# Kernel optimization log

Measured on AMD Instinct MI355X. Metric: run time of the kernel, lower is better.

The kernel has to match this reference:

```python
import jax, jax.numpy as jnp
import numpy as np


def setup_inputs() -> dict:
    key = jax.random.key(0)
    k1, k2, k3 = jax.random.split(key, 3)
    B, C, H, W = 16, 512, 64, 64
    K = 32
    std = 1.0 / (K * C) ** 0.5
    x = jax.random.normal(k1, (B, C, H, W), dtype=jnp.float32)
    codewords = jax.random.uniform(k2, (K, C), dtype=jnp.float32, minval=-std, maxval=std)
    scale = jax.random.uniform(k3, (K,), dtype=jnp.float32, minval=-1.0, maxval=0.0)
    return {"x": x, "codewords": codewords, "scale": scale}


def reference(x, codewords, scale):
    # x: [B, C, H, W] -> tokens [B, N, C] with N = H*W
    B, C, H, W = x.shape
    xf = x.reshape(B, C, H * W).transpose(0, 2, 1)  # [B, N, C]

    # (avoids materializing the [B, N, K, C] tensor the torch code builds)
    x_sq = jnp.sum(xf * xf, axis=-1)                 # [B, N]
    c_sq = jnp.sum(codewords * codewords, axis=-1)   # [K]
    xc = jnp.einsum('bnc,kc->bnk', xf, codewords)    # [B, N, K]
    scaled_l2 = scale * (x_sq[..., None] - 2.0 * xc + c_sq)  # [B, N, K]

    w = jax.nn.softmax(scaled_l2, axis=2)            # [B, N, K]

    # aggregate: sum_n w[b,n,k] * (x[b,n,:] - c[k,:])
    #          = einsum(w, x) - (sum_n w) * c
    enc = jnp.einsum('bnk,bnc->bkc', w, xf) - jnp.sum(w, axis=1)[..., None] * codewords
    return enc  # [B, K, C]
```

## Files before the change

### kernel.cpp

```cpp
#include <hip/hip_runtime.h>


#define B_ 16
#define C_ 512
#define N_ 4096
#define K_ 32
#define CHUNK 128
#define NCH (N_ / CHUNK)
#define NBLK (B_ * NCH)
#define WLS 40

typedef __attribute__((ext_vector_type(8))) short short8;
typedef __attribute__((ext_vector_type(16))) float floatx16;

__device__ inline unsigned short f2bf(float f) {
    union { float f; unsigned u; } v; v.f = f;
    unsigned r = v.u + 0x7FFFu + ((v.u >> 16) & 1u);
    return (unsigned short)(r >> 16);
}

__device__ inline void cbar() {
    __builtin_amdgcn_sched_barrier(0);
    asm volatile("s_waitcnt lgkmcnt(0)" ::: "memory");
    __builtin_amdgcn_s_barrier();
    __builtin_amdgcn_sched_barrier(0);
}

template <int USE_WS>
__global__ __launch_bounds__(256, 3)
void enc_kernel(const float* __restrict__ x,
                const float* __restrict__ cw,
                const float* __restrict__ scale,
                float* __restrict__ outp)
{
    __shared__ unsigned short Wl[4][K_ * WLS];
    __shared__ float csq[K_];
    __shared__ float scl[K_];

    const int tid  = threadIdx.x;
    const int wave = tid >> 6;
    const int lane = tid & 63;
    const int l31  = lane & 31;
    const int lh   = lane >> 5;

    const int b     = blockIdx.x >> 5;
    const int chunk = blockIdx.x & (NCH - 1);
    const float* xb = x + (long)b * C_ * N_;

    if (tid < K_) scl[tid] = scale[tid];
    {
        const int k = tid >> 3, q = tid & 7;
        const float4* src = (const float4*)(cw + k * C_ + q * 64);
        float ssum = 0.f;
        #pragma unroll
        for (int i = 0; i < 16; ++i) {
            const float4 v = src[i];
            ssum += v.x*v.x + v.y*v.y + v.z*v.z + v.w*v.w;
        }
        ssum += __shfl_xor(ssum, 1);
        ssum += __shfl_xor(ssum, 2);
        ssum += __shfl_xor(ssum, 4);
        if (q == 0) csq[k] = ssum;
    }

    const float* xcol = xb + chunk * CHUNK + wave * 32 + l31;
    const float* cwr  = cw + l31 * C_ + lh * 8;

    short8 afA[4], afB[4];
#define AFLOADG(buf_, ptr_)                                                    \
    { _Pragma("unroll")                                                        \
      for (int s = 0; s < 4; ++s) {                                            \
          const float4 u0 = *(const float4*)((ptr_) + s * 16);                 \
          const float4 u1 = *(const float4*)((ptr_) + s * 16 + 4);             \
          short8 t_;                                                           \
          t_[0] = (short)f2bf(u0.x); t_[1] = (short)f2bf(u0.y);                \
          t_[2] = (short)f2bf(u0.z); t_[3] = (short)f2bf(u0.w);                \
          t_[4] = (short)f2bf(u1.x); t_[5] = (short)f2bf(u1.y);                \
          t_[6] = (short)f2bf(u1.z); t_[7] = (short)f2bf(u1.w);                \
          buf_[s] = t_; } }

    floatx16 S;
    #pragma unroll
    for (int i = 0; i < 16; ++i) S[i] = 0.f;
    float xs = 0.f;

    AFLOADG(afA, cwr)
    #pragma unroll 2
    for (int g = 0; g < 8; ++g) {
        const float* xg = xcol + (long)g * 64 * N_;
        if (g + 1 < 8) {
            if (g & 1) AFLOADG(afA, cwr + (g + 1) * 64)
            else       AFLOADG(afB, cwr + (g + 1) * 64)
        }
        #pragma unroll
        for (int s = 0; s < 4; ++s) {
            float xv[8];
            #pragma unroll
            for (int j = 0; j < 8; ++j)
                xv[j] = xg[(long)(s * 16 + lh * 8 + j) * N_];
            short8 bx;
            #pragma unroll
            for (int j = 0; j < 8; ++j) {
                xs += xv[j] * xv[j];
                bx[j] = (short)f2bf(xv[j]);
            }
            S = __builtin_amdgcn_mfma_f32_32x32x16_bf16(
                    (g & 1) ? afB[s] : afA[s], bx, S, 0, 0, 0);
        }
    }

    xs += __shfl_xor(xs, 32);

    float4 bv[6][2];
#define G2LOAD(bi_, i_)                                                        \
    { const int t_ = (i_) >> 3, st_ = (i_) & 7;                                \
      const int c_ = wave * 128 + t_ * 32 + l31;                               \
      const int no_ = (st_ >> 1) * 32 + (st_ & 1) * 16 + lh * 8;               \
      const float* p_ = xb + (long)c_ * N_ + chunk * CHUNK + no_;              \
      bv[bi_][0] = *(const float4*)p_;                                         \
      bv[bi_][1] = *(const float4*)(p_ + 4); }
    G2LOAD(0, 0)
    G2LOAD(1, 1)
    G2LOAD(2, 2)
    G2LOAD(3, 3)
    G2LOAD(4, 4)
    G2LOAD(5, 5)

    cbar();

    {
        const float xq = xs;
        float L[16], mx = -3.4e38f;
        #pragma unroll
        for (int rr = 0; rr < 16; ++rr) {
            const int k = (rr & 3) + 8 * (rr >> 2) + 4 * lh;
            L[rr] = scl[k] * (xq - 2.f * S[rr] + csq[k]);
            mx = fmaxf(mx, L[rr]);
        }
        mx = fmaxf(mx, __shfl_xor(mx, 32));
        float sum = 0.f;
        #pragma unroll
        for (int rr = 0; rr < 16; ++rr) { L[rr] = __expf(L[rr] - mx); sum += L[rr]; }
        sum += __shfl_xor(sum, 32);
        const float inv = 1.f / sum;
        #pragma unroll
        for (int rr = 0; rr < 16; ++rr) {
            const int k = (rr & 3) + 8 * (rr >> 2) + 4 * lh;
            Wl[wave][k * WLS + l31] = f2bf(L[rr] * inv);
        }
    }
    cbar();

    short8 aw[8];
    #pragma unroll
    for (int st = 0; st < 8; ++st)
        aw[st] = *(const short8*)&Wl[st >> 1][l31 * WLS + (st & 1) * 16 + lh * 8];

    floatx16 wacc;
    #pragma unroll
    for (int i = 0; i < 16; ++i) wacc[i] = 0.f;
    {
        short8 ones;
        #pragma unroll
        for (int j = 0; j < 8; ++j) ones[j] = (short)0x3F80;
        #pragma unroll
        for (int st = 0; st < 8; ++st)
            wacc = __builtin_amdgcn_mfma_f32_32x32x16_bf16(aw[st], ones, wacc, 0, 0, 0);
    }

    floatx16 acc[4];
    #pragma unroll
    for (int t = 0; t < 4; ++t)
        #pragma unroll
        for (int i = 0; i < 16; ++i) acc[t][i] = 0.f;

    #pragma unroll
    for (int i = 0; i < 32; ++i) {
        const int bi = i % 6;
        const int t  = i >> 3, st = i & 7;
        const float4 v0 = bv[bi][0];
        const float4 v1 = bv[bi][1];
        short8 bx;
        bx[0] = (short)f2bf(v0.x); bx[1] = (short)f2bf(v0.y);
        bx[2] = (short)f2bf(v0.z); bx[3] = (short)f2bf(v0.w);
        bx[4] = (short)f2bf(v1.x); bx[5] = (short)f2bf(v1.y);
        bx[6] = (short)f2bf(v1.z); bx[7] = (short)f2bf(v1.w);
        acc[t] = __builtin_amdgcn_mfma_f32_32x32x16_bf16(aw[st], bx, acc[t], 0, 0, 0);
        if (i + 6 < 32) G2LOAD(bi, i + 6)
    }

    float* dst = USE_WS ? (outp + (size_t)blockIdx.x * K_ * C_)
                        : (outp + (size_t)b * K_ * C_);
    #pragma unroll
    for (int t = 0; t < 4; ++t) {
        const int c = wave * 128 + t * 32 + l31;
        #pragma unroll
        for (int rr = 0; rr < 16; ++rr) {
            const int k = (rr & 3) + 8 * (rr >> 2) + 4 * lh;
            const float val = acc[t][rr] - wacc[rr] * cw[k * C_ + c];
            if (USE_WS) dst[k * C_ + c] = val;
            else        atomicAdd(dst + k * C_ + c, val);
        }
    }
}

__global__ __launch_bounds__(256)
void reduce_kernel(const float4* __restrict__ part, float4* __restrict__ out)
{
    const int gid = blockIdx.x * 256 + threadIdx.x;
    const int bb  = gid >> 12;
    const int i4  = gid & 4095;
    const float4* pp = part + ((size_t)bb * NCH) * 4096 + i4;
    float4 s = make_float4(0.f, 0.f, 0.f, 0.f);
    #pragma unroll
    for (int j = 0; j < NCH; ++j) {
        const float4 v = pp[(size_t)j * 4096];
        s.x += v.x; s.y += v.y; s.z += v.z; s.w += v.w;
    }
    out[gid] = s;
}

extern "C" void kernel_launch(void* const* d_in, const int* in_sizes, int n_in,
                              void* d_out, int out_size, void* d_ws, size_t ws_size,
                              hipStream_t stream) {
    const float* x     = (const float*)d_in[0];
    const float* cw    = (const float*)d_in[1];
    const float* scale = (const float*)d_in[2];
    float* out = (float*)d_out;

    const size_t ws_need = (size_t)NBLK * K_ * C_ * sizeof(float);
    if (ws_size >= ws_need) {
        float* part = (float*)d_ws;
        hipLaunchKernelGGL(enc_kernel<1>, dim3(NBLK), dim3(256), 0, stream,
                           x, cw, scale, part);
        hipLaunchKernelGGL(reduce_kernel, dim3(256), dim3(256), 0, stream,
                           (const float4*)part, (float4*)out);
    } else {
        hipMemsetAsync(out, 0, (size_t)out_size * sizeof(float), stream);
        hipLaunchKernelGGL(enc_kernel<0>, dim3(NBLK), dim3(256), 0, stream,
                           x, cw, scale, out);
    }
}
```

Measured before the change: 223.3 us.

## Stage x slabs through double-buffered LDS with async global_load_lds

Replaces the per-lane strided scalar global loads of x in the distance GEMM phase with async global_load_lds transfers of 64-channel slabs into a double-buffered shared-memory buffer. An explicit vmcnt wait plus barriers overlaps fetching the next slab with the MFMA work on the current one. The 64KB of extra LDS forces occupancy down from 3 to 2 blocks per CU, which reduces latency hiding across blocks. It also adds two barriers per iteration.

Result: no change. 220.6 us (-1.2%).

```diff
diff --git a/kernel.cpp b/kernel.cpp
--- a/kernel.cpp
+++ b/kernel.cpp
@@ -26,13 +26,20 @@
     __builtin_amdgcn_sched_barrier(0);
 }
 
+__device__ inline void wait_vm8() {
+    __builtin_amdgcn_sched_barrier(0);
+    asm volatile("s_waitcnt vmcnt(8)" ::: "memory");
+    __builtin_amdgcn_sched_barrier(0);
+}
+
 template <int USE_WS>
-__global__ __launch_bounds__(256, 3)
+__global__ __launch_bounds__(256, 2)
 void enc_kernel(const float* __restrict__ x,
                 const float* __restrict__ cw,
                 const float* __restrict__ scale,
                 float* __restrict__ outp)
 {
+    __shared__ float slabF[2][64 * CHUNK];
     __shared__ unsigned short Wl[4][K_ * WLS];
     __shared__ float csq[K_];
     __shared__ float scl[K_];
@@ -47,6 +54,21 @@
     const int chunk = blockIdx.x & (NCH - 1);
     const float* xb = x + (long)b * C_ * N_;
 
+#define SLAB_ISSUE(p_, g_)                                                     \
+    { _Pragma("unroll")                                                        \
+      for (int m = 0; m < 8; ++m) {                                            \
+          const float* gsrc_ = xb                                              \
+              + (long)((g_) * 64 + m * 8 + wave * 2 + lh) * N_                 \
+              + chunk * CHUNK + l31 * 4;                                       \
+          __builtin_amdgcn_global_load_lds(                                    \
+              (const __attribute__((address_space(1))) unsigned int*)gsrc_,    \
+              (__attribute__((address_space(3))) unsigned int*)                \
+                  &slabF[p_][(m * 8 + wave * 2) * CHUNK],                      \
+              16, 0, 0);                                                       \
+      } }
+
+    SLAB_ISSUE(0, 0)
+
     if (tid < K_) scl[tid] = scale[tid];
     {
         const int k = tid >> 3, q = tid & 7;
@@ -63,9 +85,7 @@
         if (q == 0) csq[k] = ssum;
     }
 
-    const float* xcol = xb + chunk * CHUNK + wave * 32 + l31;
-    const float* cwr  = cw + l31 * C_ + lh * 8;
-
+    const float* cwr = cw + l31 * C_ + lh * 8;
     short8 afA[4], afB[4];
 #define AFLOADG(buf_, ptr_)                                                    \
     { _Pragma("unroll")                                                        \
@@ -79,30 +99,32 @@
           t_[6] = (short)f2bf(u1.z); t_[7] = (short)f2bf(u1.w);                \
           buf_[s] = t_; } }
 
+    AFLOADG(afA, cwr)
+
     floatx16 S;
     #pragma unroll
     for (int i = 0; i < 16; ++i) S[i] = 0.f;
     float xs = 0.f;
 
-    AFLOADG(afA, cwr)
-    #pragma unroll 2
+    #pragma unroll
     for (int g = 0; g < 8; ++g) {
-        const float* xg = xcol + (long)g * 64 * N_;
+        cbar();
+        if (g + 1 < 8) SLAB_ISSUE((g + 1) & 1, g + 1)
+        wait_vm8();
+        cbar();
         if (g + 1 < 8) {
             if (g & 1) AFLOADG(afA, cwr + (g + 1) * 64)
             else       AFLOADG(afB, cwr + (g + 1) * 64)
         }
         #pragma unroll
         for (int s = 0; s < 4; ++s) {
-            float xv[8];
-            #pragma unroll
-            for (int j = 0; j < 8; ++j)
-                xv[j] = xg[(long)(s * 16 + lh * 8 + j) * N_];
             short8 bx;
             #pragma unroll
             for (int j = 0; j < 8; ++j) {
-                xs += xv[j] * xv[j];
-                bx[j] = (short)f2bf(xv[j]);
+                const float xv = slabF[g & 1][(s * 16 + lh * 8 + j) * CHUNK
+                                              + wave * 32 + l31];
+                xs += xv * xv;
+                bx[j] = (short)f2bf(xv);
             }
             S = __builtin_amdgcn_mfma_f32_32x32x16_bf16(
                     (g & 1) ? afB[s] : afA[s], bx, S, 0, 0, 0);
@@ -126,8 +148,6 @@
     G2LOAD(4, 4)
     G2LOAD(5, 5)
 
-    cbar();
-
     {
         const float xq = xs;
         float L[16], mx = -3.4e38f;
```

## Stage x tile through LDS with coalesced loads and halve chunk size

Applied to the files above, without the earlier changes.

The token chunk per block shrinks from 128 to 64, doubling the grid. The x tile for the distance GEMM is now loaded with coalesced float4 row reads, converted to bf16 and staged in shared memory. The channel reduction is split across two wave halves, which exchange partial dot products and squared norms through LDS. This targets the strided per-element global loads of the first GEMM and raises parallelism. In exchange it doubles the partial-sum workspace that the reduce kernel must write and read, and adds several barriers.

After: 277.9 us. 1.24x slower.

```diff
diff --git a/kernel.cpp b/kernel.cpp
--- a/kernel.cpp
+++ b/kernel.cpp
@@ -5,9 +5,10 @@
 #define C_ 512
 #define N_ 4096
 #define K_ 32
-#define CHUNK 128
+#define CHUNK 64
 #define NCH (N_ / CHUNK)
 #define NBLK (B_ * NCH)
+#define XCN 68
 #define WLS 40
 
 typedef __attribute__((ext_vector_type(8))) short short8;
@@ -33,7 +34,10 @@
                 const float* __restrict__ scale,
                 float* __restrict__ outp)
 {
-    __shared__ unsigned short Wl[4][K_ * WLS];
+    __shared__ unsigned short XC[256 * XCN];
+    __shared__ float Sp[2][K_ * 32];
+    __shared__ float xsqL[16][CHUNK];
+    __shared__ unsigned short Wl[2][K_ * WLS];
     __shared__ float csq[K_];
     __shared__ float scl[K_];
 
@@ -42,36 +46,42 @@
     const int lane = tid & 63;
     const int l31  = lane & 31;
     const int lh   = lane >> 5;
-
-    const int b     = blockIdx.x >> 5;
+    const int half = wave >> 1;
+    const int tile = wave & 1;
+
+    const int b     = blockIdx.x >> 6;
     const int chunk = blockIdx.x & (NCH - 1);
     const float* xb = x + (long)b * C_ * N_;
 
-    if (tid < K_) scl[tid] = scale[tid];
-    {
-        const int k = tid >> 3, q = tid & 7;
-        const float4* src = (const float4*)(cw + k * C_ + q * 64);
-        float ssum = 0.f;
-        #pragma unroll
-        for (int i = 0; i < 16; ++i) {
-            const float4 v = src[i];
-            ssum += v.x*v.x + v.y*v.y + v.z*v.z + v.w*v.w;
-        }
-        ssum += __shfl_xor(ssum, 1);
-        ssum += __shfl_xor(ssum, 2);
-        ssum += __shfl_xor(ssum, 4);
-        if (q == 0) csq[k] = ssum;
-    }
-
-    const float* xcol = xb + chunk * CHUNK + wave * 32 + l31;
-    const float* cwr  = cw + l31 * C_ + lh * 8;
-
+    const int r = tid >> 4;
+    const int p = tid & 15;
+    const float* xrow = xb + chunk * CHUNK + p * 4;
+
+    float4 bufA[16], bufB[16];
+#define BISSUE(buf_, cbase_)                                                   \
+    { _Pragma("unroll")                                                        \
+      for (int i = 0; i < 16; ++i)                                             \
+          buf_[i] = *(const float4*)(xrow + (long)((cbase_) + i * 16 + r) * N_); }
+
+    float xs0 = 0.f, xs1 = 0.f, xs2 = 0.f, xs3 = 0.f;
+#define BWRITE(buf_)                                                           \
+    { _Pragma("unroll")                                                        \
+      for (int i = 0; i < 16; ++i) {                                           \
+          const float4 v = buf_[i];                                            \
+          xs0 += v.x * v.x; xs1 += v.y * v.y;                                  \
+          xs2 += v.z * v.z; xs3 += v.w * v.w;                                  \
+          const unsigned lo = (unsigned)f2bf(v.x) | ((unsigned)f2bf(v.y) << 16);\
+          const unsigned hi = (unsigned)f2bf(v.z) | ((unsigned)f2bf(v.w) << 16);\
+          *(uint2*)&XC[(i * 16 + r) * XCN + p * 4] = make_uint2(lo, hi);       \
+      } }
+
+    const float* cwr = cw + l31 * C_ + lh * 8;
     short8 afA[4], afB[4];
-#define AFLOADG(buf_, ptr_)                                                    \
+#define AFLOADG(buf_, coff_)                                                   \
     { _Pragma("unroll")                                                        \
       for (int s = 0; s < 4; ++s) {                                            \
-          const float4 u0 = *(const float4*)((ptr_) + s * 16);                 \
-          const float4 u1 = *(const float4*)((ptr_) + s * 16 + 4);             \
+          const float4 u0 = *(const float4*)(cwr + (coff_) + s * 16);          \
+          const float4 u1 = *(const float4*)(cwr + (coff_) + s * 16 + 4);      \
           short8 t_;                                                           \
           t_[0] = (short)f2bf(u0.x); t_[1] = (short)f2bf(u0.y);                \
           t_[2] = (short)f2bf(u0.z); t_[3] = (short)f2bf(u0.w);                \
@@ -79,62 +89,96 @@
           t_[6] = (short)f2bf(u1.z); t_[7] = (short)f2bf(u1.w);                \
           buf_[s] = t_; } }
 
+#define G1STEP(afbuf_, lg_)                                                    \
+    { _Pragma("unroll")                                                        \
+      for (int s = 0; s < 4; ++s) {                                            \
+          short8 bx;                                                           \
+          _Pragma("unroll")                                                    \
+          for (int j = 0; j < 8; ++j)                                          \
+              bx[j] = (short)XC[((lg_) * 64 + s * 16 + lh * 8 + j) * XCN       \
+                                + tile * 32 + l31];                            \
+          S = __builtin_amdgcn_mfma_f32_32x32x16_bf16(afbuf_[s], bx, S, 0, 0, 0);\
+      } }
+
+    BISSUE(bufA, 0)
+    if (tid < K_) scl[tid] = scale[tid];
+    {
+        const int k = tid >> 3, q = tid & 7;
+        const float4* src = (const float4*)(cw + k * C_ + q * 64);
+        float ssum = 0.f;
+        #pragma unroll
+        for (int i = 0; i < 16; ++i) {
+            const float4 v = src[i];
+            ssum += v.x*v.x + v.y*v.y + v.z*v.z + v.w*v.w;
+        }
+        ssum += __shfl_xor(ssum, 1);
+        ssum += __shfl_xor(ssum, 2);
+        ssum += __shfl_xor(ssum, 4);
+        if (q == 0) csq[k] = ssum;
+    }
+    AFLOADG(afA, half * 256)
+
+    BWRITE(bufA)
+    BISSUE(bufB, 256)
+    cbar();
+
     floatx16 S;
     #pragma unroll
     for (int i = 0; i < 16; ++i) S[i] = 0.f;
-    float xs = 0.f;
-
-    AFLOADG(afA, cwr)
-    #pragma unroll 2
-    for (int g = 0; g < 8; ++g) {
-        const float* xg = xcol + (long)g * 64 * N_;
-        if (g + 1 < 8) {
-            if (g & 1) AFLOADG(afA, cwr + (g + 1) * 64)
-            else       AFLOADG(afB, cwr + (g + 1) * 64)
-        }
-        #pragma unroll
-        for (int s = 0; s < 4; ++s) {
-            float xv[8];
-            #pragma unroll
-            for (int j = 0; j < 8; ++j)
-                xv[j] = xg[(long)(s * 16 + lh * 8 + j) * N_];
-            short8 bx;
-            #pragma unroll
-            for (int j = 0; j < 8; ++j) {
-                xs += xv[j] * xv[j];
-                bx[j] = (short)f2bf(xv[j]);
-            }
-            S = __builtin_amdgcn_mfma_f32_32x32x16_bf16(
-                    (g & 1) ? afB[s] : afA[s], bx, S, 0, 0, 0);
-        }
-    }
-
-    xs += __shfl_xor(xs, 32);
+
+    if (half == 0) {
+        AFLOADG(afB, 64)
+        G1STEP(afA, 0)
+        AFLOADG(afA, 128)
+        G1STEP(afB, 1)
+        AFLOADG(afB, 192)
+        G1STEP(afA, 2)
+        G1STEP(afB, 3)
+    }
+    cbar();
+
+    BWRITE(bufB)
+    xsqL[r][p * 4 + 0] = xs0; xsqL[r][p * 4 + 1] = xs1;
+    xsqL[r][p * 4 + 2] = xs2; xsqL[r][p * 4 + 3] = xs3;
+    cbar();
+
+    if (half == 1) {
+        AFLOADG(afB, 256 + 64)
+        G1STEP(afA, 0)
+        AFLOADG(afA, 256 + 128)
+        G1STEP(afB, 1)
+        AFLOADG(afB, 256 + 192)
+        G1STEP(afA, 2)
+        G1STEP(afB, 3)
+        #pragma unroll
+        for (int rr = 0; rr < 16; ++rr)
+            Sp[tile][((rr & 3) + 8 * (rr >> 2) + 4 * lh) * 32 + l31] = S[rr];
+    }
 
     float4 bv[6][2];
 #define G2LOAD(bi_, i_)                                                        \
-    { const int t_ = (i_) >> 3, st_ = (i_) & 7;                                \
+    { const int t_ = (i_) >> 2, st_ = (i_) & 3;                                \
       const int c_ = wave * 128 + t_ * 32 + l31;                               \
-      const int no_ = (st_ >> 1) * 32 + (st_ & 1) * 16 + lh * 8;               \
+      const int no_ = st_ * 16 + lh * 8;                                       \
       const float* p_ = xb + (long)c_ * N_ + chunk * CHUNK + no_;              \
       bv[bi_][0] = *(const float4*)p_;                                         \
       bv[bi_][1] = *(const float4*)(p_ + 4); }
-    G2LOAD(0, 0)
-    G2LOAD(1, 1)
-    G2LOAD(2, 2)
-    G2LOAD(3, 3)
-    G2LOAD(4, 4)
-    G2LOAD(5, 5)
-
-    cbar();
-
-    {
-        const float xq = xs;
+    if (half == 0) {
+        G2LOAD(0, 0) G2LOAD(1, 1) G2LOAD(2, 2)
+        G2LOAD(3, 3) G2LOAD(4, 4) G2LOAD(5, 5)
+    }
+    cbar();
+
+    if (half == 0) {
+        const int n = tile * 32 + l31;
+        float xq = 0.f;
+        #pragma unroll
+        for (int rr = 0; rr < 16; ++rr) xq += xsqL[rr][n];
         float L[16], mx = -3.4e38f;
         #pragma unroll
         for (int rr = 0; rr < 16; ++rr) {
             const int k = (rr & 3) + 8 * (rr >> 2) + 4 * lh;
-            L[rr] = scl[k] * (xq - 2.f * S[rr] + csq[k]);
+            L[rr] = scl[k] * (xq - 2.f * (S[rr] + Sp[tile][k * 32 + l31]) + csq[k]);
             mx = fmaxf(mx, L[rr]);
         }
         mx = fmaxf(mx, __shfl_xor(mx, 32));
@@ -146,14 +190,17 @@
         #pragma unroll
         for (int rr = 0; rr < 16; ++rr) {
             const int k = (rr & 3) + 8 * (rr >> 2) + 4 * lh;
-            Wl[wave][k * WLS + l31] = f2bf(L[rr] * inv);
-        }
-    }
-    cbar();
-
-    short8 aw[8];
-    #pragma unroll
-    for (int st = 0; st < 8; ++st)
+            Wl[tile][k * WLS + l31] = f2bf(L[rr] * inv);
+        }
+    } else {
+        G2LOAD(0, 0) G2LOAD(1, 1) G2LOAD(2, 2)
+        G2LOAD(3, 3) G2LOAD(4, 4) G2LOAD(5, 5)
+    }
+    cbar();
+
+    short8 aw[4];
+    #pragma unroll
+    for (int st = 0; st < 4; ++st)
         aw[st] = *(const short8*)&Wl[st >> 1][l31 * WLS + (st & 1) * 16 + lh * 8];
 
     floatx16 wacc;
@@ -164,7 +211,7 @@
         #pragma unroll
         for (int j = 0; j < 8; ++j) ones[j] = (short)0x3F80;
         #pragma unroll
-        for (int st = 0; st < 8; ++st)
+        for (int st = 0; st < 4; ++st)
             wacc = __builtin_amdgcn_mfma_f32_32x32x16_bf16(aw[st], ones, wacc, 0, 0, 0);
     }
 
@@ -175,9 +222,9 @@
         for (int i = 0; i < 16; ++i) acc[t][i] = 0.f;
 
     #pragma unroll
-    for (int i = 0; i < 32; ++i) {
+    for (int i = 0; i < 16; ++i) {
         const int bi = i % 6;
-        const int t  = i >> 3, st = i & 7;
+        const int t  = i >> 2, st = i & 3;
         const float4 v0 = bv[bi][0];
         const float4 v1 = bv[bi][1];
         short8 bx;
@@ -186,7 +233,7 @@
         bx[4] = (short)f2bf(v1.x); bx[5] = (short)f2bf(v1.y);
         bx[6] = (short)f2bf(v1.z); bx[7] = (short)f2bf(v1.w);
         acc[t] = __builtin_amdgcn_mfma_f32_32x32x16_bf16(aw[st], bx, acc[t], 0, 0, 0);
-        if (i + 6 < 32) G2LOAD(bi, i + 6)
+        if (i + 6 < 16) G2LOAD(bi, i + 6)
     }
 
     float* dst = USE_WS ? (outp + (size_t)blockIdx.x * K_ * C_)
@@ -212,7 +259,7 @@
     const int i4  = gid & 4095;
     const float4* pp = part + ((size_t)bb * NCH) * 4096 + i4;
     float4 s = make_float4(0.f, 0.f, 0.f, 0.f);
-    #pragma unroll
+    #pragma unroll 32
     for (int j = 0; j < NCH; ++j) {
         const float4 v = pp[(size_t)j * 4096];
         s.x += v.x; s.y += v.y; s.z += v.z; s.w += v.w;
```
